# Optimization experiments

Hardware: AMD Instinct MI355X
Metric: run time of the kernel (lower is better)

## Reference

```python
import jax, jax.numpy as jnp
import numpy as np

N_NODES = 50000
N_EDGES = 800000
D = 64
LN_EPS = 1e-5


def setup_inputs() -> dict:
    key = jax.random.key(0)
    k1, k2, k3 = jax.random.split(key, 3)
    x = jax.random.normal(k1, (N_NODES, D), dtype=jnp.float32)
    edge_index = jax.random.randint(k2, (2, N_EDGES), 0, N_NODES, dtype=jnp.int64)
    # GCNConv linear weight (no bias in lin; conv bias separate), kaiming-ish scale
    W = jax.random.normal(k3, (D, D), dtype=jnp.float32) / np.sqrt(D)
    b = jnp.zeros((D,), dtype=jnp.float32)
    # LayerNorm affine params
    gamma = jnp.ones((D,), dtype=jnp.float32)
    beta = jnp.zeros((D,), dtype=jnp.float32)
    return {"x": x, "edge_index": edge_index, "W": W, "b": b, "gamma": gamma, "beta": beta}


def reference(x, edge_index, W, b, gamma, beta):
    n = x.shape[0]
    # --- GCNConv (normalize=True, improved=False, add_self_loops=True) ---
    loops = jnp.arange(n, dtype=edge_index.dtype)
    src = jnp.concatenate([edge_index[0], loops])  # message sources j
    dst = jnp.concatenate([edge_index[1], loops])  # message targets i
    ew = jnp.ones(src.shape[0], dtype=x.dtype)
    deg = jax.ops.segment_sum(ew, dst, num_segments=n)          # in-degree incl. self-loop
    dinv = jnp.where(deg > 0, jax.lax.rsqrt(jnp.where(deg > 0, deg, 1.0)), 0.0)
    norm = dinv[src] * dinv[dst]                                 # [E+N]
    xw = x @ W                                                   # [N, D]
    z = jax.ops.segment_sum(norm[:, None] * xw[src], dst, num_segments=n) + b
    # --- identity skip connection ---
    h = x + z
    # --- norm_act_drop: LayerNorm + ReLU (dropout_prob=0) ---
    mu = jnp.mean(h, axis=-1, keepdims=True)
    var = jnp.mean((h - mu) ** 2, axis=-1, keepdims=True)
    hn = (h - mu) * jax.lax.rsqrt(var + LN_EPS)
    return jax.nn.relu(hn * gamma + beta)
```

## Files before the change

kernel.cpp:

```cpp
#include <hip/hip_runtime.h>
#include <hip/hip_fp16.h>

#define N_NODES 50000
#define N_EDGES 800000
#define D 64
#define LN_EPS 1e-5f
#define CAP 48
#define NR 8
#define RSPAN ((N_NODES + NR - 1) / NR)
#define ECHUNKS 512
#define EPC ((N_EDGES + ECHUNKS - 1) / ECHUNKS)


__global__ void fill_k(const int* __restrict__ src, const int* __restrict__ dst,
                       int* __restrict__ cnt, int* __restrict__ ssrc) {
    int r = blockIdx.x & (NR - 1);
    int chunk = blockIdx.x >> 3;
    int lo = r * RSPAN;
    int hi = lo + RSPAN; if (hi > N_NODES) hi = N_NODES;
    int ebeg = chunk * EPC;
    int eend = ebeg + EPC; if (eend > N_EDGES) eend = N_EDGES;
    for (int e = ebeg + threadIdx.x; e < eend; e += 256) {
        int t = dst[e];
        if (t >= lo && t < hi) {
            int pos = atomicAdd(&cnt[t], 1);
            if (pos < CAP) ssrc[t * CAP + pos] = src[e];
        }
    }
}

__global__ __launch_bounds__(256) void gemm_xs(const float* __restrict__ x,
                                               const float* __restrict__ W,
                                               const int* __restrict__ cnt,
                                               __half* __restrict__ xs) {
    __shared__ float xlds[D * D];
    int tid = threadIdx.x;
    int row0 = blockIdx.x * 64;

    const float4* xg = (const float4*)(x + (size_t)row0 * D);
    float4* xl4 = (float4*)xlds;
    for (int i = tid; i < D * D / 4; i += 256) {
        int grow = row0 + (i >> 4);
        xl4[i] = (grow < N_NODES) ? xg[i] : make_float4(0.f, 0.f, 0.f, 0.f);
    }

    int lane = tid & 63;
    float wcol[D];
#pragma unroll
    for (int k = 0; k < D; ++k) wcol[k] = W[k * D + lane];
    __syncthreads();

    int wv = tid >> 6;
    for (int rr = 0; rr < 16; ++rr) {
        int r = wv * 16 + rr;
        int grow = row0 + r;
        if (grow >= N_NODES) break;
        const float4* xr = (const float4*)(xlds + r * D);
        float acc = 0.f;
#pragma unroll
        for (int k4 = 0; k4 < 16; ++k4) {
            float4 xv = xr[k4];
            acc += xv.x * wcol[k4 * 4 + 0];
            acc += xv.y * wcol[k4 * 4 + 1];
            acc += xv.z * wcol[k4 * 4 + 2];
            acc += xv.w * wcol[k4 * 4 + 3];
        }
        float di = rsqrtf((float)cnt[grow] + 1.0f);
        xs[(size_t)grow * D + lane] = __float2half(di * acc);
    }
}

__global__ void agg_ln_k(const float* __restrict__ x, const __half* __restrict__ xs,
                         const int* __restrict__ cnt, const int* __restrict__ ssrc,
                         const float* __restrict__ b, const float* __restrict__ gamma,
                         const float* __restrict__ beta, float* __restrict__ out) {
    int row = blockIdx.x * 4 + (threadIdx.x >> 6);
    if (row >= N_NODES) return;
    int lane = threadIdx.x & 63;
    int sub = lane >> 3;
    int c8  = lane & 7;

    int dc = cnt[row];
    int deg = dc < CAP ? dc : CAP;
    size_t base = (size_t)row * CAP;

    float4 a0 = make_float4(0.f, 0.f, 0.f, 0.f);
    float4 a1 = make_float4(0.f, 0.f, 0.f, 0.f);
    for (int j = sub; j < deg; j += 8) {
        int s = ssrc[base + j];
        float4 raw = *(const float4*)(xs + (size_t)s * D + c8 * 8);
        const __half2* hp = (const __half2*)&raw;
        float2 p0 = __half22float2(hp[0]);
        float2 p1 = __half22float2(hp[1]);
        float2 p2 = __half22float2(hp[2]);
        float2 p3 = __half22float2(hp[3]);
        a0.x += p0.x; a0.y += p0.y; a0.z += p1.x; a0.w += p1.y;
        a1.x += p2.x; a1.y += p2.y; a1.z += p3.x; a1.w += p3.y;
    }
#pragma unroll
    for (int o = 8; o < 64; o <<= 1) {
        a0.x += __shfl_xor(a0.x, o, 64); a0.y += __shfl_xor(a0.y, o, 64);
        a0.z += __shfl_xor(a0.z, o, 64); a0.w += __shfl_xor(a0.w, o, 64);
        a1.x += __shfl_xor(a1.x, o, 64); a1.y += __shfl_xor(a1.y, o, 64);
        a1.z += __shfl_xor(a1.z, o, 64); a1.w += __shfl_xor(a1.w, o, 64);
    }

    float di = rsqrtf((float)dc + 1.0f);
    float4 sraw = *(const float4*)(xs + (size_t)row * D + c8 * 8);
    const __half2* sp = (const __half2*)&sraw;
    float2 s0 = __half22float2(sp[0]);
    float2 s1 = __half22float2(sp[1]);
    float2 s2 = __half22float2(sp[2]);
    float2 s3 = __half22float2(sp[3]);

    const float4* xp = (const float4*)(x + (size_t)row * D + c8 * 8);
    float4 x0 = xp[0], x1 = xp[1];
    const float4* bp = (const float4*)(b + c8 * 8);
    float4 b0 = bp[0], b1 = bp[1];

    float h[8];
    h[0] = x0.x + di * (a0.x + s0.x) + b0.x;
    h[1] = x0.y + di * (a0.y + s0.y) + b0.y;
    h[2] = x0.z + di * (a0.z + s1.x) + b0.z;
    h[3] = x0.w + di * (a0.w + s1.y) + b0.w;
    h[4] = x1.x + di * (a1.x + s2.x) + b1.x;
    h[5] = x1.y + di * (a1.y + s2.y) + b1.y;
    h[6] = x1.z + di * (a1.z + s3.x) + b1.z;
    h[7] = x1.w + di * (a1.w + s3.y) + b1.w;

    float s_ = 0.f;
#pragma unroll
    for (int i = 0; i < 8; ++i) s_ += h[i];
#pragma unroll
    for (int o = 1; o < 64; o <<= 1) s_ += __shfl_xor(s_, o, 64);
    float mu = s_ * (1.0f / 512.0f);
    float v_ = 0.f;
    float dd[8];
#pragma unroll
    for (int i = 0; i < 8; ++i) { dd[i] = h[i] - mu; v_ += dd[i] * dd[i]; }
#pragma unroll
    for (int o = 1; o < 64; o <<= 1) v_ += __shfl_xor(v_, o, 64);
    float rstd = rsqrtf(v_ * (1.0f / 512.0f) + LN_EPS);

    if (sub == 0) {
        const float4* gp = (const float4*)(gamma + c8 * 8);
        const float4* ep = (const float4*)(beta + c8 * 8);
        float4 g0 = gp[0], g1 = gp[1];
        float4 e0 = ep[0], e1 = ep[1];
        float4 r0, r1;
        r0.x = fmaxf(dd[0] * rstd * g0.x + e0.x, 0.f);
        r0.y = fmaxf(dd[1] * rstd * g0.y + e0.y, 0.f);
        r0.z = fmaxf(dd[2] * rstd * g0.z + e0.z, 0.f);
        r0.w = fmaxf(dd[3] * rstd * g0.w + e0.w, 0.f);
        r1.x = fmaxf(dd[4] * rstd * g1.x + e1.x, 0.f);
        r1.y = fmaxf(dd[5] * rstd * g1.y + e1.y, 0.f);
        r1.z = fmaxf(dd[6] * rstd * g1.z + e1.z, 0.f);
        r1.w = fmaxf(dd[7] * rstd * g1.w + e1.w, 0.f);
        float4* op = (float4*)(out + (size_t)row * D + c8 * 8);
        op[0] = r0;
        op[1] = r1;
    }
}

extern "C" void kernel_launch(void* const* d_in, const int* in_sizes, int n_in,
                              void* d_out, int out_size, void* d_ws, size_t ws_size,
                              hipStream_t stream) {
    const float* x     = (const float*)d_in[0];
    const int*   ei    = (const int*)d_in[1];
    const float* W     = (const float*)d_in[2];
    const float* b     = (const float*)d_in[3];
    const float* gamma = (const float*)d_in[4];
    const float* beta  = (const float*)d_in[5];
    float* out = (float*)d_out;

    const int* src = ei;
    const int* dst = ei + N_EDGES;

    int*    cnt  = (int*)d_ws;
    __half* xs   = (__half*)(cnt + N_NODES);
    int*    ssrc = (int*)(xs + (size_t)N_NODES * D);

    hipMemsetAsync(cnt, 0, N_NODES * sizeof(int), stream);
    fill_k<<<NR * ECHUNKS, 256, 0, stream>>>(src, dst, cnt, ssrc);
    gemm_xs<<<(N_NODES + 63) / 64, 256, 0, stream>>>(x, W, cnt, xs);
    agg_ln_k<<<(N_NODES + 3) / 4, 256, 0, stream>>>(x, xs, cnt, ssrc, b, gamma, beta, out);
}
```

Baseline: 162.6 us.

## Aggregate scaled features before the GEMM and fuse GEMM with LayerNorm

Reorders the GCN computation to aggregate normalized input features first and apply W afterwards, using (A X) W = A (X W). A new elementwise kernel writes a degree-scaled fp16 copy of x. A single fused kernel then gathers neighbours into shared memory, multiplies by W, and applies the residual, bias, LayerNorm and ReLU. This removes one full-feature intermediate pass. Neighbour indices are also stored as 16-bit values to shrink the adjacency buffer, which relies on the node count staying below 65536. In exchange, each wave now processes 16 rows of gathers one after another, and the W registers plus shared memory may lower occupancy for a latency-bound gather.

```diff
diff --git a/kernel.cpp b/kernel.cpp
--- a/kernel.cpp
+++ b/kernel.cpp
@@ -13,7 +13,7 @@
 
 
 __global__ void fill_k(const int* __restrict__ src, const int* __restrict__ dst,
-                       int* __restrict__ cnt, int* __restrict__ ssrc) {
+                       int* __restrict__ cnt, unsigned short* __restrict__ ssrc) {
     int r = blockIdx.x & (NR - 1);
     int chunk = blockIdx.x >> 3;
     int lo = r * RSPAN;
@@ -24,141 +24,110 @@
         int t = dst[e];
         if (t >= lo && t < hi) {
             int pos = atomicAdd(&cnt[t], 1);
-            if (pos < CAP) ssrc[t * CAP + pos] = src[e];
+            if (pos < CAP) ssrc[(size_t)t * CAP + pos] = (unsigned short)src[e];
         }
     }
 }
 
-__global__ __launch_bounds__(256) void gemm_xs(const float* __restrict__ x,
-                                               const float* __restrict__ W,
-                                               const int* __restrict__ cnt,
-                                               __half* __restrict__ xs) {
-    __shared__ float xlds[D * D];
+__global__ void prep_k(const float* __restrict__ x, const int* __restrict__ cnt,
+                       __half* __restrict__ xh) {
+    int i = blockIdx.x * 256 + threadIdx.x;
+    if (i < N_NODES * D / 4) {
+        int row = i >> 4;
+        float di = rsqrtf((float)cnt[row] + 1.0f);
+        float4 v = ((const float4*)x)[i];
+        __half2* o = (__half2*)xh + (size_t)i * 2;
+        o[0] = __floats2half2_rn(di * v.x, di * v.y);
+        o[1] = __floats2half2_rn(di * v.z, di * v.w);
+    }
+}
+
+__global__ __launch_bounds__(256) void fused_k(
+        const float* __restrict__ x, const __half* __restrict__ xh,
+        const int* __restrict__ cnt, const unsigned short* __restrict__ ssrc,
+        const float* __restrict__ W, const float* __restrict__ b,
+        const float* __restrict__ gamma, const float* __restrict__ beta,
+        float* __restrict__ out) {
+    __shared__ float y[D * D];
     int tid = threadIdx.x;
+    int lane = tid & 63;
+    int wv = tid >> 6;
     int row0 = blockIdx.x * 64;
 
-    const float4* xg = (const float4*)(x + (size_t)row0 * D);
-    float4* xl4 = (float4*)xlds;
-    for (int i = tid; i < D * D / 4; i += 256) {
-        int grow = row0 + (i >> 4);
-        xl4[i] = (grow < N_NODES) ? xg[i] : make_float4(0.f, 0.f, 0.f, 0.f);
+    int sub = lane >> 3;
+    int c8 = lane & 7;
+    for (int rr = 0; rr < 16; ++rr) {
+        int row = row0 + wv * 16 + rr;
+        float4 a0 = make_float4(0.f, 0.f, 0.f, 0.f);
+        float4 a1 = make_float4(0.f, 0.f, 0.f, 0.f);
+        if (row < N_NODES) {
+            int dc = cnt[row];
+            int deg = dc < CAP ? dc : CAP;
+            size_t base = (size_t)row * CAP;
+            if (sub == 0) {
+                float4 raw = *(const float4*)(xh + (size_t)row * D + c8 * 8);
+                const __half2* hp = (const __half2*)&raw;
+                float2 p0 = __half22float2(hp[0]), p1 = __half22float2(hp[1]);
+                float2 p2 = __half22float2(hp[2]), p3 = __half22float2(hp[3]);
+                a0.x += p0.x; a0.y += p0.y; a0.z += p1.x; a0.w += p1.y;
+                a1.x += p2.x; a1.y += p2.y; a1.z += p3.x; a1.w += p3.y;
+            }
+            for (int j = sub; j < deg; j += 8) {
+                int s = ssrc[base + j];
+                float4 raw = *(const float4*)(xh + (size_t)s * D + c8 * 8);
+                const __half2* hp = (const __half2*)&raw;
+                float2 p0 = __half22float2(hp[0]), p1 = __half22float2(hp[1]);
+                float2 p2 = __half22float2(hp[2]), p3 = __half22float2(hp[3]);
+                a0.x += p0.x; a0.y += p0.y; a0.z += p1.x; a0.w += p1.y;
+                a1.x += p2.x; a1.y += p2.y; a1.z += p3.x; a1.w += p3.y;
+            }
+        }
+#pragma unroll
+        for (int o = 8; o < 64; o <<= 1) {
+            a0.x += __shfl_xor(a0.x, o, 64); a0.y += __shfl_xor(a0.y, o, 64);
+            a0.z += __shfl_xor(a0.z, o, 64); a0.w += __shfl_xor(a0.w, o, 64);
+            a1.x += __shfl_xor(a1.x, o, 64); a1.y += __shfl_xor(a1.y, o, 64);
+            a1.z += __shfl_xor(a1.z, o, 64); a1.w += __shfl_xor(a1.w, o, 64);
+        }
+        if (sub == 0) {
+            float* yr = y + (wv * 16 + rr) * D + c8 * 8;
+            *(float4*)yr = a0;
+            *(float4*)(yr + 4) = a1;
+        }
     }
 
-    int lane = tid & 63;
     float wcol[D];
 #pragma unroll
     for (int k = 0; k < D; ++k) wcol[k] = W[k * D + lane];
+    float bl = b[lane], gl = gamma[lane], el = beta[lane];
     __syncthreads();
 
-    int wv = tid >> 6;
     for (int rr = 0; rr < 16; ++rr) {
         int r = wv * 16 + rr;
         int grow = row0 + r;
         if (grow >= N_NODES) break;
-        const float4* xr = (const float4*)(xlds + r * D);
+        const float4* yr = (const float4*)(y + r * D);
         float acc = 0.f;
 #pragma unroll
         for (int k4 = 0; k4 < 16; ++k4) {
-            float4 xv = xr[k4];
-            acc += xv.x * wcol[k4 * 4 + 0];
-            acc += xv.y * wcol[k4 * 4 + 1];
-            acc += xv.z * wcol[k4 * 4 + 2];
-            acc += xv.w * wcol[k4 * 4 + 3];
+            float4 v = yr[k4];
+            acc += v.x * wcol[k4 * 4 + 0];
+            acc += v.y * wcol[k4 * 4 + 1];
+            acc += v.z * wcol[k4 * 4 + 2];
+            acc += v.w * wcol[k4 * 4 + 3];
         }
         float di = rsqrtf((float)cnt[grow] + 1.0f);
-        xs[(size_t)grow * D + lane] = __float2half(di * acc);
-    }
-}
-
-__global__ void agg_ln_k(const float* __restrict__ x, const __half* __restrict__ xs,
-                         const int* __restrict__ cnt, const int* __restrict__ ssrc,
-                         const float* __restrict__ b, const float* __restrict__ gamma,
-                         const float* __restrict__ beta, float* __restrict__ out) {
-    int row = blockIdx.x * 4 + (threadIdx.x >> 6);
-    if (row >= N_NODES) return;
-    int lane = threadIdx.x & 63;
-    int sub = lane >> 3;
-    int c8  = lane & 7;
-
-    int dc = cnt[row];
-    int deg = dc < CAP ? dc : CAP;
-    size_t base = (size_t)row * CAP;
-
-    float4 a0 = make_float4(0.f, 0.f, 0.f, 0.f);
-    float4 a1 = make_float4(0.f, 0.f, 0.f, 0.f);
-    for (int j = sub; j < deg; j += 8) {
-        int s = ssrc[base + j];
-        float4 raw = *(const float4*)(xs + (size_t)s * D + c8 * 8);
-        const __half2* hp = (const __half2*)&raw;
-        float2 p0 = __half22float2(hp[0]);
-        float2 p1 = __half22float2(hp[1]);
-        float2 p2 = __half22float2(hp[2]);
-        float2 p3 = __half22float2(hp[3]);
-        a0.x += p0.x; a0.y += p0.y; a0.z += p1.x; a0.w += p1.y;
-        a1.x += p2.x; a1.y += p2.y; a1.z += p3.x; a1.w += p3.y;
-    }
+        float h = x[(size_t)grow * D + lane] + di * acc + bl;
+        float s_ = h;
 #pragma unroll
-    for (int o = 8; o < 64; o <<= 1) {
-        a0.x += __shfl_xor(a0.x, o, 64); a0.y += __shfl_xor(a0.y, o, 64);
-        a0.z += __shfl_xor(a0.z, o, 64); a0.w += __shfl_xor(a0.w, o, 64);
-        a1.x += __shfl_xor(a1.x, o, 64); a1.y += __shfl_xor(a1.y, o, 64);
-        a1.z += __shfl_xor(a1.z, o, 64); a1.w += __shfl_xor(a1.w, o, 64);
-    }
-
-    float di = rsqrtf((float)dc + 1.0f);
-    float4 sraw = *(const float4*)(xs + (size_t)row * D + c8 * 8);
-    const __half2* sp = (const __half2*)&sraw;
-    float2 s0 = __half22float2(sp[0]);
-    float2 s1 = __half22float2(sp[1]);
-    float2 s2 = __half22float2(sp[2]);
-    float2 s3 = __half22float2(sp[3]);
-
-    const float4* xp = (const float4*)(x + (size_t)row * D + c8 * 8);
-    float4 x0 = xp[0], x1 = xp[1];
-    const float4* bp = (const float4*)(b + c8 * 8);
-    float4 b0 = bp[0], b1 = bp[1];
-
-    float h[8];
-    h[0] = x0.x + di * (a0.x + s0.x) + b0.x;
-    h[1] = x0.y + di * (a0.y + s0.y) + b0.y;
-    h[2] = x0.z + di * (a0.z + s1.x) + b0.z;
-    h[3] = x0.w + di * (a0.w + s1.y) + b0.w;
-    h[4] = x1.x + di * (a1.x + s2.x) + b1.x;
-    h[5] = x1.y + di * (a1.y + s2.y) + b1.y;
-    h[6] = x1.z + di * (a1.z + s3.x) + b1.z;
-    h[7] = x1.w + di * (a1.w + s3.y) + b1.w;
-
-    float s_ = 0.f;
+        for (int o = 1; o < 64; o <<= 1) s_ += __shfl_xor(s_, o, 64);
+        float mu = s_ * (1.0f / D);
+        float d = h - mu;
+        float v_ = d * d;
 #pragma unroll
-    for (int i = 0; i < 8; ++i) s_ += h[i];
-#pragma unroll
-    for (int o = 1; o < 64; o <<= 1) s_ += __shfl_xor(s_, o, 64);
-    float mu = s_ * (1.0f / 512.0f);
-    float v_ = 0.f;
-    float dd[8];
-#pragma unroll
-    for (int i = 0; i < 8; ++i) { dd[i] = h[i] - mu; v_ += dd[i] * dd[i]; }
-#pragma unroll
-    for (int o = 1; o < 64; o <<= 1) v_ += __shfl_xor(v_, o, 64);
-    float rstd = rsqrtf(v_ * (1.0f / 512.0f) + LN_EPS);
-
-    if (sub == 0) {
-        const float4* gp = (const float4*)(gamma + c8 * 8);
-        const float4* ep = (const float4*)(beta + c8 * 8);
-        float4 g0 = gp[0], g1 = gp[1];
-        float4 e0 = ep[0], e1 = ep[1];
-        float4 r0, r1;
-        r0.x = fmaxf(dd[0] * rstd * g0.x + e0.x, 0.f);
-        r0.y = fmaxf(dd[1] * rstd * g0.y + e0.y, 0.f);
-        r0.z = fmaxf(dd[2] * rstd * g0.z + e0.z, 0.f);
-        r0.w = fmaxf(dd[3] * rstd * g0.w + e0.w, 0.f);
-        r1.x = fmaxf(dd[4] * rstd * g1.x + e1.x, 0.f);
-        r1.y = fmaxf(dd[5] * rstd * g1.y + e1.y, 0.f);
-        r1.z = fmaxf(dd[6] * rstd * g1.z + e1.z, 0.f);
-        r1.w = fmaxf(dd[7] * rstd * g1.w + e1.w, 0.f);
-        float4* op = (float4*)(out + (size_t)row * D + c8 * 8);
-        op[0] = r0;
-        op[1] = r1;
+        for (int o = 1; o < 64; o <<= 1) v_ += __shfl_xor(v_, o, 64);
+        float rstd = rsqrtf(v_ * (1.0f / D) + LN_EPS);
+        out[(size_t)grow * D + lane] = fmaxf(d * rstd * gl + el, 0.f);
     }
 }
 
@@ -176,12 +145,12 @@
     const int* src = ei;
     const int* dst = ei + N_EDGES;
 
-    int*    cnt  = (int*)d_ws;
-    __half* xs   = (__half*)(cnt + N_NODES);
-    int*    ssrc = (int*)(xs + (size_t)N_NODES * D);
+    int*            cnt  = (int*)d_ws;
+    __half*         xh   = (__half*)(cnt + N_NODES);
+    unsigned short* ssrc = (unsigned short*)(xh + (size_t)N_NODES * D);
 
     hipMemsetAsync(cnt, 0, N_NODES * sizeof(int), stream);
     fill_k<<<NR * ECHUNKS, 256, 0, stream>>>(src, dst, cnt, ssrc);
-    gemm_xs<<<(N_NODES + 63) / 64, 256, 0, stream>>>(x, W, cnt, xs);
-    agg_ln_k<<<(N_NODES + 3) / 4, 256, 0, stream>>>(x, xs, cnt, ssrc, b, gamma, beta, out);
+    prep_k<<<(N_NODES * D / 4 + 255) / 256, 256, 0, stream>>>(x, cnt, xh);
+    fused_k<<<(N_NODES + 63) / 64, 256, 0, stream>>>(x, xh, cnt, ssrc, W, b, gamma, beta, out);
 }
```

New measurement: 178.5 us. 9.8% more time.

## Compress edge indices to 16-bit and unroll neighbor gather with preloaded indices

Applied to the files above, without the earlier changes.

Adds a prep kernel that zeroes the degree counters, replacing the separate memset, and packs src/dst edge indices into 16-bit arrays. This works because node ids fit below 65536. fill_k rescans the edge list once per range, and the neighbor list is now stored as u16, so index traffic roughly halves in both fill_k and the aggregation. The aggregation kernel preloads up to six neighbor indices per lane and folds the self-loop into a fully unrolled gather loop, to expose more concurrent loads. The cost is an extra kernel pass over the edge list, and the code now depends on the node count staying below 65536.

```diff
diff --git a/kernel.cpp b/kernel.cpp
--- a/kernel.cpp
+++ b/kernel.cpp
@@ -11,9 +11,26 @@
 #define ECHUNKS 512
 #define EPC ((N_EDGES + ECHUNKS - 1) / ECHUNKS)
 
-
-__global__ void fill_k(const int* __restrict__ src, const int* __restrict__ dst,
-                       int* __restrict__ cnt, int* __restrict__ ssrc) {
+typedef unsigned short u16;
+
+
+__global__ void prep_edges_k(const int* __restrict__ src, const int* __restrict__ dst,
+                             u16* __restrict__ usrc, u16* __restrict__ udst,
+                             int* __restrict__ cnt) {
+    int gid = blockIdx.x * 256 + threadIdx.x;
+    if (gid < N_NODES) cnt[gid] = 0;
+    if (gid < N_EDGES / 4) {
+        int4 s = ((const int4*)src)[gid];
+        int4 d = ((const int4*)dst)[gid];
+        ((uint2*)usrc)[gid] = make_uint2((unsigned)(u16)s.x | ((unsigned)(u16)s.y << 16),
+                                         (unsigned)(u16)s.z | ((unsigned)(u16)s.w << 16));
+        ((uint2*)udst)[gid] = make_uint2((unsigned)(u16)d.x | ((unsigned)(u16)d.y << 16),
+                                         (unsigned)(u16)d.z | ((unsigned)(u16)d.w << 16));
+    }
+}
+
+__global__ void fill_k(const u16* __restrict__ usrc, const u16* __restrict__ udst,
+                       int* __restrict__ cnt, u16* __restrict__ ssrc) {
     int r = blockIdx.x & (NR - 1);
     int chunk = blockIdx.x >> 3;
     int lo = r * RSPAN;
@@ -21,10 +38,10 @@
     int ebeg = chunk * EPC;
     int eend = ebeg + EPC; if (eend > N_EDGES) eend = N_EDGES;
     for (int e = ebeg + threadIdx.x; e < eend; e += 256) {
-        int t = dst[e];
+        int t = udst[e];
         if (t >= lo && t < hi) {
             int pos = atomicAdd(&cnt[t], 1);
-            if (pos < CAP) ssrc[t * CAP + pos] = src[e];
+            if (pos < CAP) ssrc[(size_t)t * CAP + pos] = usrc[e];
         }
     }
 }
@@ -71,7 +88,7 @@
 }
 
 __global__ void agg_ln_k(const float* __restrict__ x, const __half* __restrict__ xs,
-                         const int* __restrict__ cnt, const int* __restrict__ ssrc,
+                         const int* __restrict__ cnt, const u16* __restrict__ ssrc,
                          const float* __restrict__ b, const float* __restrict__ gamma,
                          const float* __restrict__ beta, float* __restrict__ out) {
     int row = blockIdx.x * 4 + (threadIdx.x >> 6);
@@ -84,18 +101,26 @@
     int deg = dc < CAP ? dc : CAP;
     size_t base = (size_t)row * CAP;
 
+    int sv[7];
+    int nr = (deg > sub) ? ((deg - sub + 7) >> 3) : 0;
+#pragma unroll
+    for (int r2 = 0; r2 < 6; ++r2)
+        if (r2 < nr) sv[r2] = ssrc[base + sub + (r2 << 3)];
+    if (sub == 0) { sv[nr] = row; ++nr; }
+
     float4 a0 = make_float4(0.f, 0.f, 0.f, 0.f);
     float4 a1 = make_float4(0.f, 0.f, 0.f, 0.f);
-    for (int j = sub; j < deg; j += 8) {
-        int s = ssrc[base + j];
-        float4 raw = *(const float4*)(xs + (size_t)s * D + c8 * 8);
-        const __half2* hp = (const __half2*)&raw;
-        float2 p0 = __half22float2(hp[0]);
-        float2 p1 = __half22float2(hp[1]);
-        float2 p2 = __half22float2(hp[2]);
-        float2 p3 = __half22float2(hp[3]);
-        a0.x += p0.x; a0.y += p0.y; a0.z += p1.x; a0.w += p1.y;
-        a1.x += p2.x; a1.y += p2.y; a1.z += p3.x; a1.w += p3.y;
+#pragma unroll
+    for (int r2 = 0; r2 < 7; ++r2) {
+        if (r2 < nr) {
+            int s = sv[r2];
+            float4 raw = *(const float4*)(xs + (size_t)s * D + c8 * 8);
+            const __half2* hp = (const __half2*)&raw;
+            float2 p0 = __half22float2(hp[0]), p1 = __half22float2(hp[1]);
+            float2 p2 = __half22float2(hp[2]), p3 = __half22float2(hp[3]);
+            a0.x += p0.x; a0.y += p0.y; a0.z += p1.x; a0.w += p1.y;
+            a1.x += p2.x; a1.y += p2.y; a1.z += p3.x; a1.w += p3.y;
+        }
     }
 #pragma unroll
     for (int o = 8; o < 64; o <<= 1) {
@@ -106,12 +131,6 @@
     }
 
     float di = rsqrtf((float)dc + 1.0f);
-    float4 sraw = *(const float4*)(xs + (size_t)row * D + c8 * 8);
-    const __half2* sp = (const __half2*)&sraw;
-    float2 s0 = __half22float2(sp[0]);
-    float2 s1 = __half22float2(sp[1]);
-    float2 s2 = __half22float2(sp[2]);
-    float2 s3 = __half22float2(sp[3]);
 
     const float4* xp = (const float4*)(x + (size_t)row * D + c8 * 8);
     float4 x0 = xp[0], x1 = xp[1];
@@ -119,14 +138,14 @@
     float4 b0 = bp[0], b1 = bp[1];
 
     float h[8];
-    h[0] = x0.x + di * (a0.x + s0.x) + b0.x;
-    h[1] = x0.y + di * (a0.y + s0.y) + b0.y;
-    h[2] = x0.z + di * (a0.z + s1.x) + b0.z;
-    h[3] = x0.w + di * (a0.w + s1.y) + b0.w;
-    h[4] = x1.x + di * (a1.x + s2.x) + b1.x;
-    h[5] = x1.y + di * (a1.y + s2.y) + b1.y;
-    h[6] = x1.z + di * (a1.z + s3.x) + b1.z;
-    h[7] = x1.w + di * (a1.w + s3.y) + b1.w;
+    h[0] = x0.x + di * a0.x + b0.x;
+    h[1] = x0.y + di * a0.y + b0.y;
+    h[2] = x0.z + di * a0.z + b0.z;
+    h[3] = x0.w + di * a0.w + b0.w;
+    h[4] = x1.x + di * a1.x + b1.x;
+    h[5] = x1.y + di * a1.y + b1.y;
+    h[6] = x1.z + di * a1.z + b1.z;
+    h[7] = x1.w + di * a1.w + b1.w;
 
     float s_ = 0.f;
 #pragma unroll
@@ -178,10 +197,12 @@
 
     int*    cnt  = (int*)d_ws;
     __half* xs   = (__half*)(cnt + N_NODES);
-    int*    ssrc = (int*)(xs + (size_t)N_NODES * D);
-
-    hipMemsetAsync(cnt, 0, N_NODES * sizeof(int), stream);
-    fill_k<<<NR * ECHUNKS, 256, 0, stream>>>(src, dst, cnt, ssrc);
+    u16*    usrc = (u16*)(xs + (size_t)N_NODES * D);
+    u16*    udst = usrc + N_EDGES;
+    u16*    ssrc = udst + N_EDGES;
+
+    prep_edges_k<<<(N_EDGES / 4 + 255) / 256, 256, 0, stream>>>(src, dst, usrc, udst, cnt);
+    fill_k<<<NR * ECHUNKS, 256, 0, stream>>>(usrc, udst, cnt, ssrc);
     gemm_xs<<<(N_NODES + 63) / 64, 256, 0, stream>>>(x, W, cnt, xs);
     agg_ln_k<<<(N_NODES + 3) / 4, 256, 0, stream>>>(x, xs, cnt, ssrc, b, gamma, beta, out);
 }
```

Result: no change. 162.1 us (-0.3%).

## Bucket edges by group in a single pass with 16-bit source indices

Applied to the files above, without the earlier changes.

The edge-fill kernel now reads each edge once and scatters it into one of 8 per-block-group buckets. Before, each of 8 node-range passes re-read the whole dst array. Source ids are stored as 16-bit values and loaded as uint4, so each aggregation sub-lane reads its bucket with one or two vector loads. A separate kernel sums the 8 group counts into a precomputed inverse-sqrt degree array that GEMM and aggregation both use. The cost is a larger memset, an extra launch, a 16-per-group capacity limit, and a dependence on node ids fitting in 16 bits.

```diff
diff --git a/kernel.cpp b/kernel.cpp
--- a/kernel.cpp
+++ b/kernel.cpp
@@ -5,33 +5,35 @@
 #define N_EDGES 800000
 #define D 64
 #define LN_EPS 1e-5f
-#define CAP 48
-#define NR 8
-#define RSPAN ((N_NODES + NR - 1) / NR)
-#define ECHUNKS 512
-#define EPC ((N_EDGES + ECHUNKS - 1) / ECHUNKS)
+#define NG 8
+#define CAP_G 16
+
+typedef unsigned short u16;
 
 
 __global__ void fill_k(const int* __restrict__ src, const int* __restrict__ dst,
-                       int* __restrict__ cnt, int* __restrict__ ssrc) {
-    int r = blockIdx.x & (NR - 1);
-    int chunk = blockIdx.x >> 3;
-    int lo = r * RSPAN;
-    int hi = lo + RSPAN; if (hi > N_NODES) hi = N_NODES;
-    int ebeg = chunk * EPC;
-    int eend = ebeg + EPC; if (eend > N_EDGES) eend = N_EDGES;
-    for (int e = ebeg + threadIdx.x; e < eend; e += 256) {
-        int t = dst[e];
-        if (t >= lo && t < hi) {
-            int pos = atomicAdd(&cnt[t], 1);
-            if (pos < CAP) ssrc[t * CAP + pos] = src[e];
-        }
-    }
+                       int* __restrict__ cnt8, u16* __restrict__ ssrc) {
+    int e = blockIdx.x * 256 + threadIdx.x;
+    if (e >= N_EDGES) return;
+    int g = blockIdx.x & (NG - 1);
+    int t = dst[e];
+    int pos = atomicAdd(&cnt8[g * N_NODES + t], 1);
+    if (pos < CAP_G)
+        ssrc[((size_t)g * N_NODES + t) * CAP_G + pos] = (u16)src[e];
+}
+
+__global__ void di_k(const int* __restrict__ cnt8, float* __restrict__ di) {
+    int i = blockIdx.x * 256 + threadIdx.x;
+    if (i >= N_NODES) return;
+    int d = 0;
+#pragma unroll
+    for (int g = 0; g < NG; ++g) d += cnt8[g * N_NODES + i];
+    di[i] = rsqrtf((float)d + 1.0f);
 }
 
 __global__ __launch_bounds__(256) void gemm_xs(const float* __restrict__ x,
                                                const float* __restrict__ W,
-                                               const int* __restrict__ cnt,
+                                               const float* __restrict__ di,
                                                __half* __restrict__ xs) {
     __shared__ float xlds[D * D];
     int tid = threadIdx.x;
@@ -65,38 +67,61 @@
             acc += xv.z * wcol[k4 * 4 + 2];
             acc += xv.w * wcol[k4 * 4 + 3];
         }
-        float di = rsqrtf((float)cnt[grow] + 1.0f);
-        xs[(size_t)grow * D + lane] = __float2half(di * acc);
+        xs[(size_t)grow * D + lane] = __float2half(di[grow] * acc);
     }
 }
 
 __global__ void agg_ln_k(const float* __restrict__ x, const __half* __restrict__ xs,
-                         const int* __restrict__ cnt, const int* __restrict__ ssrc,
-                         const float* __restrict__ b, const float* __restrict__ gamma,
-                         const float* __restrict__ beta, float* __restrict__ out) {
+                         const float* __restrict__ di, const int* __restrict__ cnt8,
+                         const u16* __restrict__ ssrc, const float* __restrict__ b,
+                         const float* __restrict__ gamma, const float* __restrict__ beta,
+                         float* __restrict__ out) {
     int row = blockIdx.x * 4 + (threadIdx.x >> 6);
     if (row >= N_NODES) return;
     int lane = threadIdx.x & 63;
     int sub = lane >> 3;
     int c8  = lane & 7;
 
-    int dc = cnt[row];
-    int deg = dc < CAP ? dc : CAP;
-    size_t base = (size_t)row * CAP;
+    int cg = cnt8[sub * N_NODES + row];
+    int deg_g = cg < CAP_G ? cg : CAP_G;
+    const uint4* bck = (const uint4*)(ssrc + ((size_t)sub * N_NODES + row) * CAP_G);
 
     float4 a0 = make_float4(0.f, 0.f, 0.f, 0.f);
     float4 a1 = make_float4(0.f, 0.f, 0.f, 0.f);
-    for (int j = sub; j < deg; j += 8) {
-        int s = ssrc[base + j];
-        float4 raw = *(const float4*)(xs + (size_t)s * D + c8 * 8);
-        const __half2* hp = (const __half2*)&raw;
-        float2 p0 = __half22float2(hp[0]);
-        float2 p1 = __half22float2(hp[1]);
-        float2 p2 = __half22float2(hp[2]);
-        float2 p3 = __half22float2(hp[3]);
-        a0.x += p0.x; a0.y += p0.y; a0.z += p1.x; a0.w += p1.y;
-        a1.x += p2.x; a1.y += p2.y; a1.z += p3.x; a1.w += p3.y;
-    }
+
+#define GATHER(sid)                                                             \
+    {                                                                           \
+        float4 raw = *(const float4*)(xs + (size_t)(sid) * D + c8 * 8);         \
+        const __half2* hp = (const __half2*)&raw;                               \
+        float2 p0 = __half22float2(hp[0]), p1 = __half22float2(hp[1]);          \
+        float2 p2 = __half22float2(hp[2]), p3 = __half22float2(hp[3]);          \
+        a0.x += p0.x; a0.y += p0.y; a0.z += p1.x; a0.w += p1.y;                 \
+        a1.x += p2.x; a1.y += p2.y; a1.z += p3.x; a1.w += p3.y;                 \
+    }
+
+    if (sub == 0) GATHER(row);
+
+    if (deg_g > 0) {
+        uint4 q0 = bck[0];
+        unsigned sv[8];
+        sv[0] = q0.x & 0xffff; sv[1] = q0.x >> 16;
+        sv[2] = q0.y & 0xffff; sv[3] = q0.y >> 16;
+        sv[4] = q0.z & 0xffff; sv[5] = q0.z >> 16;
+        sv[6] = q0.w & 0xffff; sv[7] = q0.w >> 16;
+        int n0 = deg_g < 8 ? deg_g : 8;
+        for (int j = 0; j < n0; ++j) GATHER(sv[j]);
+        if (deg_g > 8) {
+            uint4 q1 = bck[1];
+            unsigned sw[8];
+            sw[0] = q1.x & 0xffff; sw[1] = q1.x >> 16;
+            sw[2] = q1.y & 0xffff; sw[3] = q1.y >> 16;
+            sw[4] = q1.z & 0xffff; sw[5] = q1.z >> 16;
+            sw[6] = q1.w & 0xffff; sw[7] = q1.w >> 16;
+            for (int j = 0; j < deg_g - 8; ++j) GATHER(sw[j]);
+        }
+    }
+#undef GATHER
+
 #pragma unroll
     for (int o = 8; o < 64; o <<= 1) {
         a0.x += __shfl_xor(a0.x, o, 64); a0.y += __shfl_xor(a0.y, o, 64);
@@ -105,13 +130,7 @@
         a1.z += __shfl_xor(a1.z, o, 64); a1.w += __shfl_xor(a1.w, o, 64);
     }
 
-    float di = rsqrtf((float)dc + 1.0f);
-    float4 sraw = *(const float4*)(xs + (size_t)row * D + c8 * 8);
-    const __half2* sp = (const __half2*)&sraw;
-    float2 s0 = __half22float2(sp[0]);
-    float2 s1 = __half22float2(sp[1]);
-    float2 s2 = __half22float2(sp[2]);
-    float2 s3 = __half22float2(sp[3]);
+    float dr = di[row];
 
     const float4* xp = (const float4*)(x + (size_t)row * D + c8 * 8);
     float4 x0 = xp[0], x1 = xp[1];
@@ -119,14 +138,14 @@
     float4 b0 = bp[0], b1 = bp[1];
 
     float h[8];
-    h[0] = x0.x + di * (a0.x + s0.x) + b0.x;
-    h[1] = x0.y + di * (a0.y + s0.y) + b0.y;
-    h[2] = x0.z + di * (a0.z + s1.x) + b0.z;
-    h[3] = x0.w + di * (a0.w + s1.y) + b0.w;
-    h[4] = x1.x + di * (a1.x + s2.x) + b1.x;
-    h[5] = x1.y + di * (a1.y + s2.y) + b1.y;
-    h[6] = x1.z + di * (a1.z + s3.x) + b1.z;
-    h[7] = x1.w + di * (a1.w + s3.y) + b1.w;
+    h[0] = x0.x + dr * a0.x + b0.x;
+    h[1] = x0.y + dr * a0.y + b0.y;
+    h[2] = x0.z + dr * a0.z + b0.z;
+    h[3] = x0.w + dr * a0.w + b0.w;
+    h[4] = x1.x + dr * a1.x + b1.x;
+    h[5] = x1.y + dr * a1.y + b1.y;
+    h[6] = x1.z + dr * a1.z + b1.z;
+    h[7] = x1.w + dr * a1.w + b1.w;
 
     float s_ = 0.f;
 #pragma unroll
@@ -176,12 +195,14 @@
     const int* src = ei;
     const int* dst = ei + N_EDGES;
 
-    int*    cnt  = (int*)d_ws;
-    __half* xs   = (__half*)(cnt + N_NODES);
-    int*    ssrc = (int*)(xs + (size_t)N_NODES * D);
-
-    hipMemsetAsync(cnt, 0, N_NODES * sizeof(int), stream);
-    fill_k<<<NR * ECHUNKS, 256, 0, stream>>>(src, dst, cnt, ssrc);
-    gemm_xs<<<(N_NODES + 63) / 64, 256, 0, stream>>>(x, W, cnt, xs);
-    agg_ln_k<<<(N_NODES + 3) / 4, 256, 0, stream>>>(x, xs, cnt, ssrc, b, gamma, beta, out);
-}
+    int*    cnt8 = (int*)d_ws;
+    float*  di   = (float*)(cnt8 + NG * N_NODES);
+    __half* xs   = (__half*)(di + N_NODES);
+    u16*    ssrc = (u16*)(xs + (size_t)N_NODES * D);
+
+    hipMemsetAsync(cnt8, 0, NG * N_NODES * sizeof(int), stream);
+    fill_k<<<(N_EDGES + 255) / 256, 256, 0, stream>>>(src, dst, cnt8, ssrc);
+    di_k<<<(N_NODES + 255) / 256, 256, 0, stream>>>(cnt8, di);
+    gemm_xs<<<(N_NODES + 63) / 64, 256, 0, stream>>>(x, W, di, xs);
+    agg_ln_k<<<(N_NODES + 3) / 4, 256, 0, stream>>>(x, xs, di, cnt8, ssrc, b, gamma, beta, out);
+}
```

New measurement: 167.4 us. 1.03x slower.
